# Performance work log

Hardware: AMD Instinct MI355X
Metric: run time of the kernel (lower is better)

The kernel has to match this reference:

```python
import jax, jax.numpy as jnp
import numpy as np

B, H, L, D = 2, 16, 2048, 64
EPS = 1e-6  # guard for all-zero causal rows after ReLU feature map


def setup_inputs() -> dict:
    key = jax.random.key(0)
    k1, k2, k3, k4, k5 = jax.random.split(key, 5)
    return {
        "query_states": jax.random.normal(k1, (B, H, L, D), dtype=jnp.float32),
        "key_states": jax.random.normal(k2, (B, H, L, D), dtype=jnp.float32),
        "value_states": jax.random.normal(k3, (B, H, L, D), dtype=jnp.float32),
        # LinearFeatureMap params: nn.Parameter(torch.rand(H, D, D)) -> uniform[0,1)
        "fm_query": jax.random.uniform(k4, (H, D, D), dtype=jnp.float32),
        "fm_key": jax.random.uniform(k5, (H, D, D), dtype=jnp.float32),
    }


def _feature_map(states, w):
    # states: [B,H,L,D]; w: [H,D,E]. Matches einsum('blhd,hde->blhe') after transposes.
    return jax.nn.relu(jnp.einsum('bhld,hde->bhle', states, w))


def reference(query_states, key_states, value_states, fm_query, fm_key):
    q = _feature_map(query_states, fm_query)   # [B,H,L,E]
    k = _feature_map(key_states, fm_key)       # [B,H,L,E]
    # quadratic (non-softmax) causal attention
    a = jnp.einsum('bhme,bhne->bhmn', q, k)    # [B,H,L,L]
    causal = jnp.tril(jnp.ones((L, L), dtype=bool))
    a = jnp.where(causal, a, 0.0)
    a = a / (jnp.sum(a, axis=-1, keepdims=True) + EPS)
    return jnp.einsum('bhmn,bhnd->bhmd', a, value_states)
```

## Files before the change

kernel.cpp:

```cpp
#include <hip/hip_runtime.h>
#include <hip/hip_bf16.h>

#define BH_  32
#define H_   16
#define L_   2048
#define D_   64
#define NC_  32
#define STR  72

typedef _Float16 half8 __attribute__((ext_vector_type(8)));
typedef _Float16 half4 __attribute__((ext_vector_type(4)));
typedef float    floatx4 __attribute__((ext_vector_type(4)));

#define MFMA(a, b, c) __builtin_amdgcn_mfma_f32_16x16x32_f16((a), (b), (c), 0, 0, 0)

__device__ __forceinline__ half8 ldfrag(const _Float16* p, int row0, int k0) {
    const int lane = threadIdx.x & 63;
    const _Float16* q = p + (row0 + (lane & 15)) * STR + k0 + ((lane >> 4) << 3);
    return *(const half8*)q;
}

__global__ __launch_bounds__(256)
void k0_weights(const float* __restrict__ Wq, const float* __restrict__ Wk,
                _Float16* __restrict__ WqTh, _Float16* __restrict__ WqTl,
                _Float16* __restrict__ WkT) {
    __shared__ float sQ[64 * 65];
    __shared__ float sK[64 * 65];
    const int h = blockIdx.x, tid = threadIdx.x;
    const float* Wqg = Wq + (size_t)h * 4096;
    const float* Wkg = Wk + (size_t)h * 4096;
    for (int i = 0; i < 16; ++i) {
        int flat = i * 256 + tid;
        int d = flat >> 6, e = flat & 63;
        sQ[e * 65 + d] = Wqg[flat];
        sK[e * 65 + d] = Wkg[flat];
    }
    __syncthreads();
    for (int i = 0; i < 4; ++i) {
        int flat = i * 1024 + tid * 4;
        int e = flat >> 6, d0 = flat & 63;
        half4 qh, ql, kh;
        #pragma unroll
        for (int j = 0; j < 4; ++j) {
            float qv = sQ[e * 65 + d0 + j];
            _Float16 hi = (_Float16)qv;
            qh[j] = hi; ql[j] = (_Float16)(qv - (float)hi);
            kh[j] = (_Float16)sK[e * 65 + d0 + j];
        }
        *(half4*)(WqTh + (size_t)h * 4096 + flat) = qh;
        *(half4*)(WqTl + (size_t)h * 4096 + flat) = ql;
        *(half4*)(WkT  + (size_t)h * 4096 + flat) = kh;
    }
}

__global__ __launch_bounds__(256, 2)
void ka_chunksum(const float* __restrict__ K, const float* __restrict__ V,
                 const _Float16* __restrict__ WkT,
                 float* __restrict__ Scs, float* __restrict__ zc,
                 _Float16* __restrict__ kf16, _Float16* __restrict__ VT16) {
    __shared__ __align__(16) _Float16 sK  [64 * STR];
    __shared__ __align__(16) _Float16 sWkT[64 * STR];
    __shared__ __align__(16) _Float16 sVT [64 * STR];
    __shared__ __align__(16) _Float16 sKfT[64 * STR];

    const int c = blockIdx.x, bh = blockIdx.y, h = bh & (H_ - 1);
    const int tid = threadIdx.x, lane = tid & 63, w = tid >> 6;
    const int quad = lane >> 4, cl = lane & 15;

    const float* Kg = K + ((size_t)bh * L_ + c * 64) * D_;
    const float* Vg = V + ((size_t)bh * L_ + c * 64) * D_;
    const size_t cb = (size_t)bh * NC_ + c;

    for (int i = 0; i < 4; ++i) {
        int flat = i * 1024 + tid * 4;
        int r = flat >> 6, e0 = flat & 63;
        float4 kv = *(const float4*)(Kg + flat);
        half4 kh = { (_Float16)kv.x, (_Float16)kv.y, (_Float16)kv.z, (_Float16)kv.w };
        *(half4*)(sK + r * STR + e0) = kh;
        float4 vv = *(const float4*)(Vg + flat);
        sVT[(e0 + 0) * STR + r] = (_Float16)vv.x;
        sVT[(e0 + 1) * STR + r] = (_Float16)vv.y;
        sVT[(e0 + 2) * STR + r] = (_Float16)vv.z;
        sVT[(e0 + 3) * STR + r] = (_Float16)vv.w;
    }
    for (int i = 0; i < 2; ++i) {
        int flat = i * 2048 + tid * 8;
        int e = flat >> 6, d0 = flat & 63;
        *(half8*)(sWkT + e * STR + d0) = *(const half8*)(WkT + (size_t)h * 4096 + flat);
    }
    __syncthreads();

    half8 ak0 = ldfrag(sK, w * 16, 0), ak1 = ldfrag(sK, w * 16, 32);
    for (int et = 0; et < 4; ++et) {
        floatx4 acc = {0.f, 0.f, 0.f, 0.f};
        acc = MFMA(ak0, ldfrag(sWkT, et * 16, 0),  acc);
        acc = MFMA(ak1, ldfrag(sWkT, et * 16, 32), acc);
        #pragma unroll
        for (int r = 0; r < 4; ++r) {
            float v = acc[r] > 0.f ? acc[r] : 0.f;
            _Float16 hv = (_Float16)v;
            int n = w * 16 + quad * 4 + r, f = et * 16 + cl;
            sKfT[f * STR + n] = hv;
            sK  [n * STR + f] = hv;
        }
    }
    __syncthreads();

    for (int i = 0; i < 2; ++i) {
        int flat = i * 2048 + tid * 8;
        int rr = flat >> 6, c0 = flat & 63;
        *(half8*)(kf16 + cb * 4096 + flat) = *(const half8*)(sK  + rr * STR + c0);
        *(half8*)(VT16 + cb * 4096 + flat) = *(const half8*)(sVT + rr * STR + c0);
    }
    if (tid < 64) {
        float s = 0.f;
        #pragma unroll
        for (int j = 0; j < 8; ++j) {
            half8 hv = *(const half8*)(sKfT + tid * STR + j * 8);
            #pragma unroll
            for (int t = 0; t < 8; ++t) s += (float)hv[t];
        }
        zc[cb * 64 + tid] = s;
    }

    float* So = Scs + cb * 4096;
    half8 av0 = ldfrag(sVT, w * 16, 0), av1 = ldfrag(sVT, w * 16, 32);
    for (int et = 0; et < 4; ++et) {
        floatx4 acc = {0.f, 0.f, 0.f, 0.f};
        acc = MFMA(av0, ldfrag(sKfT, et * 16, 0),  acc);
        acc = MFMA(av1, ldfrag(sKfT, et * 16, 32), acc);
        #pragma unroll
        for (int r = 0; r < 4; ++r)
            So[(w * 16 + quad * 4 + r) * 64 + et * 16 + cl] = acc[r];
    }
}

__global__ __launch_bounds__(64)
void kp_prefix(float* __restrict__ Scs, float* __restrict__ zc) {
    const int bid = blockIdx.x, t = threadIdx.x;
    if (bid < BH_ * 64) {
        const int bh = bid >> 6, d = bid & 63;
        size_t base = (size_t)bh * NC_ * 4096 + (size_t)d * 64 + t;
        float run = 0.f;
        #pragma unroll
        for (int c = 0; c < NC_; ++c) {
            float v = Scs[base + (size_t)c * 4096];
            Scs[base + (size_t)c * 4096] = run;
            run += v;
        }
    } else {
        const int bh = bid - BH_ * 64;
        size_t base = (size_t)bh * NC_ * 64 + t;
        float run = 0.f;
        #pragma unroll
        for (int c = 0; c < NC_; ++c) {
            float v = zc[base + c * 64];
            zc[base + c * 64] = run;
            run += v;
        }
    }
}

__global__ __launch_bounds__(256, 2)
void kb_attn(const float* __restrict__ Q, const _Float16* __restrict__ WqTh,
             const _Float16* __restrict__ WqTl, const _Float16* __restrict__ kf16,
             const _Float16* __restrict__ VT16, const float* __restrict__ Sst,
             const float* __restrict__ zs, float* __restrict__ Out) {
    __shared__ __align__(16) _Float16 sQh[64 * STR];
    __shared__ __align__(16) _Float16 sQl[64 * STR];
    __shared__ __align__(16) _Float16 sWh[64 * STR];
    __shared__ __align__(16) _Float16 sWl[64 * STR];
    __shared__ __align__(16) _Float16 sKf[64 * STR];
    __shared__ __align__(16) _Float16 sVT[64 * STR];
    __shared__ __align__(16) _Float16 sST[64 * STR];
    __shared__ float sZ[64];

    const int c = blockIdx.x, bh = blockIdx.y, h = bh & (H_ - 1);
    const int tid = threadIdx.x, lane = tid & 63, w = tid >> 6;
    const int quad = lane >> 4, cl = lane & 15;

    const float* Qg = Q + ((size_t)bh * L_ + c * 64) * D_;
    const size_t cb = (size_t)bh * NC_ + c;
    const float* Sg = Sst + cb * 4096;

    for (int i = 0; i < 4; ++i) {
        int flat = i * 1024 + tid * 4;
        int r = flat >> 6, e0 = flat & 63;
        float4 qv = *(const float4*)(Qg + flat);
        half4 qh, ql;
        #pragma unroll
        for (int j = 0; j < 4; ++j) {
            float x = (&qv.x)[j];
            _Float16 hi = (_Float16)x;
            qh[j] = hi; ql[j] = (_Float16)(x - (float)hi);
        }
        *(half4*)(sQh + r * STR + e0) = qh;
        *(half4*)(sQl + r * STR + e0) = ql;
        float4 sv = *(const float4*)(Sg + flat);
        half4 sh = { (_Float16)sv.x, (_Float16)sv.y, (_Float16)sv.z, (_Float16)sv.w };
        *(half4*)(sST + r * STR + e0) = sh;
    }
    for (int i = 0; i < 2; ++i) {
        int flat = i * 2048 + tid * 8;
        int rr = flat >> 6, c0 = flat & 63;
        *(half8*)(sWh + rr * STR + c0) = *(const half8*)(WqTh + (size_t)h * 4096 + flat);
        *(half8*)(sWl + rr * STR + c0) = *(const half8*)(WqTl + (size_t)h * 4096 + flat);
        *(half8*)(sKf + rr * STR + c0) = *(const half8*)(kf16 + cb * 4096 + flat);
        *(half8*)(sVT + rr * STR + c0) = *(const half8*)(VT16 + cb * 4096 + flat);
    }
    if (tid < 64) sZ[tid] = zs[cb * 64 + tid];
    __syncthreads();

    half8 aqh0 = ldfrag(sQh, w * 16, 0), aqh1 = ldfrag(sQh, w * 16, 32);
    half8 aql0 = ldfrag(sQl, w * 16, 0), aql1 = ldfrag(sQl, w * 16, 32);
    float dq[4] = {0.f, 0.f, 0.f, 0.f};
    for (int et = 0; et < 4; ++et) {
        half8 bh0 = ldfrag(sWh, et * 16, 0), bh1 = ldfrag(sWh, et * 16, 32);
        half8 bl0 = ldfrag(sWl, et * 16, 0), bl1 = ldfrag(sWl, et * 16, 32);
        floatx4 acc = {0.f, 0.f, 0.f, 0.f};
        acc = MFMA(aqh0, bh0, acc);
        acc = MFMA(aqh1, bh1, acc);
        acc = MFMA(aqh0, bl0, acc);
        acc = MFMA(aqh1, bl1, acc);
        acc = MFMA(aql0, bh0, acc);
        acc = MFMA(aql1, bh1, acc);
        float zv = sZ[et * 16 + cl];
        #pragma unroll
        for (int r = 0; r < 4; ++r) {
            float v = acc[r] > 0.f ? acc[r] : 0.f;
            dq[r] += v * zv;
            _Float16 hi = (_Float16)v;
            int row = w * 16 + quad * 4 + r, col = et * 16 + cl;
            sQh[row * STR + col] = hi;
            sQl[row * STR + col] = (_Float16)(v - (float)hi);
        }
    }
    #pragma unroll
    for (int r = 0; r < 4; ++r) {
        dq[r] += __shfl_xor(dq[r], 1);
        dq[r] += __shfl_xor(dq[r], 2);
        dq[r] += __shfl_xor(dq[r], 4);
        dq[r] += __shfl_xor(dq[r], 8);
    }
    __syncthreads();

    half8 qh0 = ldfrag(sQh, w * 16, 0), qh1 = ldfrag(sQh, w * 16, 32);
    half8 ql0 = ldfrag(sQl, w * 16, 0), ql1 = ldfrag(sQl, w * 16, 32);
    _Float16* P = sWl;
    float rs[4] = {0.f, 0.f, 0.f, 0.f};
    float inv[4];
    for (int nt = 0; nt <= w; ++nt) {
        half8 b0 = ldfrag(sKf, nt * 16, 0), b1 = ldfrag(sKf, nt * 16, 32);
        floatx4 acc = {0.f, 0.f, 0.f, 0.f};
        acc = MFMA(qh0, b0, acc);
        acc = MFMA(qh1, b1, acc);
        acc = MFMA(ql0, b0, acc);
        acc = MFMA(ql1, b1, acc);
        #pragma unroll
        for (int r = 0; r < 4; ++r) {
            float v = acc[r];
            if (nt == w && cl > quad * 4 + r) v = 0.f;
            rs[r] += v;
            P[(w * 16 + quad * 4 + r) * STR + nt * 16 + cl] = (_Float16)v;
        }
    }
    for (int nt = w + 1; nt < 4; ++nt) {
        #pragma unroll
        for (int r = 0; r < 4; ++r)
            P[(w * 16 + quad * 4 + r) * STR + nt * 16 + cl] = (_Float16)0.f;
    }
    #pragma unroll
    for (int r = 0; r < 4; ++r) {
        float s = rs[r];
        s += __shfl_xor(s, 1);
        s += __shfl_xor(s, 2);
        s += __shfl_xor(s, 4);
        s += __shfl_xor(s, 8);
        inv[r] = 1.f / (s + dq[r] + 1e-6f);
    }
    __syncthreads();

    half8 p0 = ldfrag(P, w * 16, 0), p1 = ldfrag(P, w * 16, 32);
    float* Og = Out + ((size_t)bh * L_ + c * 64) * D_;
    for (int et = 0; et < 4; ++et) {
        floatx4 acc = {0.f, 0.f, 0.f, 0.f};
        half8 s0 = ldfrag(sST, et * 16, 0), s1 = ldfrag(sST, et * 16, 32);
        acc = MFMA(qh0, s0, acc);
        acc = MFMA(qh1, s1, acc);
        acc = MFMA(ql0, s0, acc);
        acc = MFMA(ql1, s1, acc);
        acc = MFMA(p0, ldfrag(sVT, et * 16, 0),  acc);
        acc = MFMA(p1, ldfrag(sVT, et * 16, 32), acc);
        #pragma unroll
        for (int r = 0; r < 4; ++r)
            Og[(w * 16 + quad * 4 + r) * 64 + et * 16 + cl] = acc[r] * inv[r];
    }
}

extern "C" void kernel_launch(void* const* d_in, const int* in_sizes, int n_in,
                              void* d_out, int out_size, void* d_ws, size_t ws_size,
                              hipStream_t stream) {
    const float* Q  = (const float*)d_in[0];
    const float* K  = (const float*)d_in[1];
    const float* V  = (const float*)d_in[2];
    const float* Wq = (const float*)d_in[3];
    const float* Wk = (const float*)d_in[4];
    float* Out = (float*)d_out;

    float*    Scs  = (float*)d_ws;
    float*    zc   = Scs + (size_t)BH_ * NC_ * 4096;
    _Float16* kf16 = (_Float16*)(zc + (size_t)BH_ * NC_ * 64);
    _Float16* VT16 = kf16 + (size_t)BH_ * NC_ * 4096;
    _Float16* WqTh = VT16 + (size_t)BH_ * NC_ * 4096;
    _Float16* WqTl = WqTh + (size_t)H_ * 4096;
    _Float16* WkT  = WqTl + (size_t)H_ * 4096;

    dim3 grid(NC_, BH_);
    hipLaunchKernelGGL(k0_weights, dim3(H_), dim3(256), 0, stream, Wq, Wk, WqTh, WqTl, WkT);
    hipLaunchKernelGGL(ka_chunksum, grid, dim3(256), 0, stream, K, V, WkT, Scs, zc, kf16, VT16);
    hipLaunchKernelGGL(kp_prefix, dim3(BH_ * 64 + BH_), dim3(64), 0, stream, Scs, zc);
    hipLaunchKernelGGL(kb_attn, grid, dim3(256), 0, stream, Q, WqTh, WqTl, kf16, VT16, Scs, zc, Out);
}
```

Baseline: 121.4 us.

## Store prefix state in fp16 and drop split-precision q-feature MFMAs

The chunk state sums are now stored in fp16 instead of fp32, which halves the traffic in the chunk-sum, prefix and attention kernels. The prefix kernel now processes packed half2 pairs. The attention kernel drops the hi/lo split of the q features, which cuts MFMA count in the QK and output stages. It also reads the S and V^T fragments straight from global memory instead of staging them in LDS, removes two block barriers, and raises the occupancy hint to three blocks. In exchange, rounding the features and prefix sums to fp16 lowers accuracy and could break the tolerance on long causal sums.

```diff
diff --git a/kernel.cpp b/kernel.cpp
--- a/kernel.cpp
+++ b/kernel.cpp
@@ -10,6 +10,7 @@
 
 typedef _Float16 half8 __attribute__((ext_vector_type(8)));
 typedef _Float16 half4 __attribute__((ext_vector_type(4)));
+typedef _Float16 half2v __attribute__((ext_vector_type(2)));
 typedef float    floatx4 __attribute__((ext_vector_type(4)));
 
 #define MFMA(a, b, c) __builtin_amdgcn_mfma_f32_16x16x32_f16((a), (b), (c), 0, 0, 0)
@@ -56,7 +57,7 @@
 __global__ __launch_bounds__(256, 2)
 void ka_chunksum(const float* __restrict__ K, const float* __restrict__ V,
                  const _Float16* __restrict__ WkT,
-                 float* __restrict__ Scs, float* __restrict__ zc,
+                 _Float16* __restrict__ Ss, float* __restrict__ zc,
                  _Float16* __restrict__ kf16, _Float16* __restrict__ VT16) {
     __shared__ __align__(16) _Float16 sK  [64 * STR];
     __shared__ __align__(16) _Float16 sWkT[64 * STR];
@@ -123,7 +124,7 @@
         zc[cb * 64 + tid] = s;
     }
 
-    float* So = Scs + cb * 4096;
+    _Float16* So = Ss + cb * 4096;
     half8 av0 = ldfrag(sVT, w * 16, 0), av1 = ldfrag(sVT, w * 16, 32);
     for (int et = 0; et < 4; ++et) {
         floatx4 acc = {0.f, 0.f, 0.f, 0.f};
@@ -131,25 +132,29 @@
         acc = MFMA(av1, ldfrag(sKfT, et * 16, 32), acc);
         #pragma unroll
         for (int r = 0; r < 4; ++r)
-            So[(w * 16 + quad * 4 + r) * 64 + et * 16 + cl] = acc[r];
+            So[(w * 16 + quad * 4 + r) * 64 + et * 16 + cl] = (_Float16)acc[r];
     }
 }
 
 __global__ __launch_bounds__(64)
-void kp_prefix(float* __restrict__ Scs, float* __restrict__ zc) {
+void kp_prefix(_Float16* __restrict__ Ss, float* __restrict__ zc) {
     const int bid = blockIdx.x, t = threadIdx.x;
-    if (bid < BH_ * 64) {
-        const int bh = bid >> 6, d = bid & 63;
-        size_t base = (size_t)bh * NC_ * 4096 + (size_t)d * 64 + t;
-        float run = 0.f;
+    if (bid < BH_ * 32) {
+        const int bh = bid >> 5, dq = bid & 31;
+        uint32_t* S32 = (uint32_t*)Ss;
+        size_t base = (size_t)bh * NC_ * 2048 + dq * 64 + t;
+        float r0 = 0.f, r1 = 0.f;
         #pragma unroll
         for (int c = 0; c < NC_; ++c) {
-            float v = Scs[base + (size_t)c * 4096];
-            Scs[base + (size_t)c * 4096] = run;
-            run += v;
+            uint32_t u = S32[base + (size_t)c * 2048];
+            half2v hv = *(half2v*)&u;
+            float v0 = (float)hv[0], v1 = (float)hv[1];
+            half2v o; o[0] = (_Float16)r0; o[1] = (_Float16)r1;
+            S32[base + (size_t)c * 2048] = *(uint32_t*)&o;
+            r0 += v0; r1 += v1;
         }
     } else {
-        const int bh = bid - BH_ * 64;
+        const int bh = bid - BH_ * 32;
         size_t base = (size_t)bh * NC_ * 64 + t;
         float run = 0.f;
         #pragma unroll
@@ -161,18 +166,16 @@
     }
 }
 
-__global__ __launch_bounds__(256, 2)
+__global__ __launch_bounds__(256, 3)
 void kb_attn(const float* __restrict__ Q, const _Float16* __restrict__ WqTh,
              const _Float16* __restrict__ WqTl, const _Float16* __restrict__ kf16,
-             const _Float16* __restrict__ VT16, const float* __restrict__ Sst,
+             const _Float16* __restrict__ VT16, const _Float16* __restrict__ Ss,
              const float* __restrict__ zs, float* __restrict__ Out) {
     __shared__ __align__(16) _Float16 sQh[64 * STR];
     __shared__ __align__(16) _Float16 sQl[64 * STR];
     __shared__ __align__(16) _Float16 sWh[64 * STR];
     __shared__ __align__(16) _Float16 sWl[64 * STR];
     __shared__ __align__(16) _Float16 sKf[64 * STR];
-    __shared__ __align__(16) _Float16 sVT[64 * STR];
-    __shared__ __align__(16) _Float16 sST[64 * STR];
     __shared__ float sZ[64];
 
     const int c = blockIdx.x, bh = blockIdx.y, h = bh & (H_ - 1);
@@ -181,7 +184,8 @@
 
     const float* Qg = Q + ((size_t)bh * L_ + c * 64) * D_;
     const size_t cb = (size_t)bh * NC_ + c;
-    const float* Sg = Sst + cb * 4096;
+    const _Float16* Sgp = Ss   + cb * 4096;
+    const _Float16* Vgp = VT16 + cb * 4096;
 
     for (int i = 0; i < 4; ++i) {
         int flat = i * 1024 + tid * 4;
@@ -196,9 +200,6 @@
         }
         *(half4*)(sQh + r * STR + e0) = qh;
         *(half4*)(sQl + r * STR + e0) = ql;
-        float4 sv = *(const float4*)(Sg + flat);
-        half4 sh = { (_Float16)sv.x, (_Float16)sv.y, (_Float16)sv.z, (_Float16)sv.w };
-        *(half4*)(sST + r * STR + e0) = sh;
     }
     for (int i = 0; i < 2; ++i) {
         int flat = i * 2048 + tid * 8;
@@ -206,7 +207,6 @@
         *(half8*)(sWh + rr * STR + c0) = *(const half8*)(WqTh + (size_t)h * 4096 + flat);
         *(half8*)(sWl + rr * STR + c0) = *(const half8*)(WqTl + (size_t)h * 4096 + flat);
         *(half8*)(sKf + rr * STR + c0) = *(const half8*)(kf16 + cb * 4096 + flat);
-        *(half8*)(sVT + rr * STR + c0) = *(const half8*)(VT16 + cb * 4096 + flat);
     }
     if (tid < 64) sZ[tid] = zs[cb * 64 + tid];
     __syncthreads();
@@ -229,10 +229,7 @@
         for (int r = 0; r < 4; ++r) {
             float v = acc[r] > 0.f ? acc[r] : 0.f;
             dq[r] += v * zv;
-            _Float16 hi = (_Float16)v;
-            int row = w * 16 + quad * 4 + r, col = et * 16 + cl;
-            sQh[row * STR + col] = hi;
-            sQl[row * STR + col] = (_Float16)(v - (float)hi);
+            sQh[(w * 16 + quad * 4 + r) * STR + et * 16 + cl] = (_Float16)v;
         }
     }
     #pragma unroll
@@ -242,20 +239,15 @@
         dq[r] += __shfl_xor(dq[r], 4);
         dq[r] += __shfl_xor(dq[r], 8);
     }
-    __syncthreads();
 
     half8 qh0 = ldfrag(sQh, w * 16, 0), qh1 = ldfrag(sQh, w * 16, 32);
-    half8 ql0 = ldfrag(sQl, w * 16, 0), ql1 = ldfrag(sQl, w * 16, 32);
-    _Float16* P = sWl;
+    _Float16* P = sQl;
     float rs[4] = {0.f, 0.f, 0.f, 0.f};
     float inv[4];
     for (int nt = 0; nt <= w; ++nt) {
-        half8 b0 = ldfrag(sKf, nt * 16, 0), b1 = ldfrag(sKf, nt * 16, 32);
-        floatx4 acc = {0.f, 0.f, 0.f, 0.f};
-        acc = MFMA(qh0, b0, acc);
-        acc = MFMA(qh1, b1, acc);
-        acc = MFMA(ql0, b0, acc);
-        acc = MFMA(ql1, b1, acc);
+        floatx4 acc = {0.f, 0.f, 0.f, 0.f};
+        acc = MFMA(qh0, ldfrag(sKf, nt * 16, 0),  acc);
+        acc = MFMA(qh1, ldfrag(sKf, nt * 16, 32), acc);
         #pragma unroll
         for (int r = 0; r < 4; ++r) {
             float v = acc[r];
@@ -278,19 +270,21 @@
         s += __shfl_xor(s, 8);
         inv[r] = 1.f / (s + dq[r] + 1e-6f);
     }
-    __syncthreads();
 
     half8 p0 = ldfrag(P, w * 16, 0), p1 = ldfrag(P, w * 16, 32);
     float* Og = Out + ((size_t)bh * L_ + c * 64) * D_;
     for (int et = 0; et < 4; ++et) {
-        floatx4 acc = {0.f, 0.f, 0.f, 0.f};
-        half8 s0 = ldfrag(sST, et * 16, 0), s1 = ldfrag(sST, et * 16, 32);
+        const _Float16* srow = Sgp + (et * 16 + cl) * 64 + quad * 8;
+        const _Float16* vrow = Vgp + (et * 16 + cl) * 64 + quad * 8;
+        half8 s0 = *(const half8*)(srow);
+        half8 s1 = *(const half8*)(srow + 32);
+        half8 v0 = *(const half8*)(vrow);
+        half8 v1 = *(const half8*)(vrow + 32);
+        floatx4 acc = {0.f, 0.f, 0.f, 0.f};
         acc = MFMA(qh0, s0, acc);
         acc = MFMA(qh1, s1, acc);
-        acc = MFMA(ql0, s0, acc);
-        acc = MFMA(ql1, s1, acc);
-        acc = MFMA(p0, ldfrag(sVT, et * 16, 0),  acc);
-        acc = MFMA(p1, ldfrag(sVT, et * 16, 32), acc);
+        acc = MFMA(p0,  v0, acc);
+        acc = MFMA(p1,  v1, acc);
         #pragma unroll
         for (int r = 0; r < 4; ++r)
             Og[(w * 16 + quad * 4 + r) * 64 + et * 16 + cl] = acc[r] * inv[r];
@@ -307,8 +301,8 @@
     const float* Wk = (const float*)d_in[4];
     float* Out = (float*)d_out;
 
-    float*    Scs  = (float*)d_ws;
-    float*    zc   = Scs + (size_t)BH_ * NC_ * 4096;
+    _Float16* Ss   = (_Float16*)d_ws;
+    float*    zc   = (float*)(Ss + (size_t)BH_ * NC_ * 4096);
     _Float16* kf16 = (_Float16*)(zc + (size_t)BH_ * NC_ * 64);
     _Float16* VT16 = kf16 + (size_t)BH_ * NC_ * 4096;
     _Float16* WqTh = VT16 + (size_t)BH_ * NC_ * 4096;
@@ -317,7 +311,7 @@
 
     dim3 grid(NC_, BH_);
     hipLaunchKernelGGL(k0_weights, dim3(H_), dim3(256), 0, stream, Wq, Wk, WqTh, WqTl, WkT);
-    hipLaunchKernelGGL(ka_chunksum, grid, dim3(256), 0, stream, K, V, WkT, Scs, zc, kf16, VT16);
-    hipLaunchKernelGGL(kp_prefix, dim3(BH_ * 64 + BH_), dim3(64), 0, stream, Scs, zc);
-    hipLaunchKernelGGL(kb_attn, grid, dim3(256), 0, stream, Q, WqTh, WqTl, kf16, VT16, Scs, zc, Out);
-}
+    hipLaunchKernelGGL(ka_chunksum, grid, dim3(256), 0, stream, K, V, WkT, Ss, zc, kf16, VT16);
+    hipLaunchKernelGGL(kp_prefix, dim3(BH_ * 32 + BH_), dim3(64), 0, stream, Ss, zc);
+    hipLaunchKernelGGL(kb_attn, grid, dim3(256), 0, stream, Q, WqTh, WqTl, kf16, VT16, Ss, zc, Out);
+}
```

Result: no change. 120.6 us (-0.7%).
